# Optimization experiments

Measured on AMD Instinct MI355X. Metric: run time of the kernel, lower is better.

The kernel has to match this reference:

```python
import jax, jax.numpy as jnp
import numpy as np

N_NODES = 50000
N_EDGES = 800000
IN_DIM = 256
OUT_DIM = 64
HEADS = 4
NEG_SLOPE = 0.2  # PyG GATConv default


def setup_inputs() -> dict:
    key = jax.random.key(0)
    k1, k2, k3, k4, k5, k6 = jax.random.split(key, 6)
    x = jax.random.normal(k1, (N_NODES, IN_DIM), dtype=jnp.float32)
    edge_index = jax.random.randint(k2, (2, N_EDGES), 0, N_NODES, dtype=jnp.int64)
    scale = 1.0 / np.sqrt(IN_DIM)
    W = jax.random.normal(k3, (IN_DIM, HEADS * OUT_DIM), dtype=jnp.float32) * scale
    att_src = jax.random.normal(k4, (HEADS, OUT_DIM), dtype=jnp.float32) * scale
    att_dst = jax.random.normal(k5, (HEADS, OUT_DIM), dtype=jnp.float32) * scale
    bias = jnp.zeros((HEADS * OUT_DIM,), dtype=jnp.float32)
    return {"x": x, "edge_index": edge_index, "W": W,
            "att_src": att_src, "att_dst": att_dst, "bias": bias}


def reference(x, edge_index, W, att_src, att_dst, bias):
    N = x.shape[0]
    H, C = att_src.shape
    # add self loops (PyG GATConv default add_self_loops=True)
    loop = jnp.arange(N, dtype=edge_index.dtype)
    src = jnp.concatenate([edge_index[0], loop])  # [E+N] source j
    dst = jnp.concatenate([edge_index[1], loop])  # [E+N] target i
    # linear projection, per-head features  [N, H, C]
    h = (x @ W).reshape(N, H, C)
    # attention logits: a_src . h_j + a_dst . h_i  -> [E, H]
    a_src = jnp.einsum('nhc,hc->nh', h, att_src)
    a_dst = jnp.einsum('nhc,hc->nh', h, att_dst)
    e = jax.nn.leaky_relu(a_src[src] + a_dst[dst], negative_slope=NEG_SLOPE)
    # edge softmax over incoming edges of each destination node
    m = jax.ops.segment_max(e, dst, num_segments=N)          # [N, H]
    p = jnp.exp(e - m[dst])                                  # [E, H]
    denom = jax.ops.segment_sum(p, dst, num_segments=N)      # [N, H]
    alpha = p / (denom[dst] + 1e-16)                         # [E, H]
    # weighted scatter-aggregate of gathered source features
    out = jax.ops.segment_sum(alpha[:, :, None] * h[src], dst, num_segments=N)
    out = out.reshape(N, H * C) + bias
    return jax.nn.relu(out)  # GATLayer active_func
```

## Files before the change

kernel.cpp:

```cpp
#include <hip/hip_runtime.h>

constexpr int N  = 50000;
constexpr int E  = 800000;
constexpr int K  = 256;
constexpr int F  = 256;
constexpr int H  = 4;
constexpr float SLOPE = 0.2f;

constexpr int WT_ROWS = 272;

constexpr size_t OFF_HB   = 0;
constexpr size_t OFF_WT   = OFF_HB   + (size_t)N * F * 2;
constexpr size_t OFF_ASRC = OFF_WT   + (size_t)WT_ROWS * K * 2;
constexpr size_t OFF_ADST = OFF_ASRC + (size_t)N * H * 4;
constexpr size_t OFF_DEG  = OFF_ADST + (size_t)N * H * 4;
constexpr size_t OFF_OFFS = OFF_DEG  + (size_t)N * 4;
constexpr size_t OFF_FLAG = OFF_OFFS + (size_t)(N + 16) * 4;
constexpr size_t OFF_RANK = OFF_FLAG + 64;
constexpr size_t OFF_CSR  = OFF_RANK + (size_t)E * 4;

constexpr int HIST_BLOCKS = 128;
constexpr int GEMM_BLOCKS = (N + 127) / 128;

typedef short short8 __attribute__((ext_vector_type(8)));
typedef float floatx4 __attribute__((ext_vector_type(4)));

__device__ __forceinline__ float leaky(float x) {
    return x > 0.f ? x : SLOPE * x;
}
__device__ __forceinline__ float blo(unsigned u) { return __uint_as_float(u << 16); }
__device__ __forceinline__ float bhi(unsigned u) { return __uint_as_float(u & 0xffff0000u); }
__device__ __forceinline__ unsigned short f2b(float f) {
    unsigned u = __float_as_uint(f);
    return (unsigned short)((u + 0x7fffu + ((u >> 16) & 1u)) >> 16);
}
__device__ __forceinline__ unsigned pk2(float a, float b) {
    return (unsigned)f2b(a) | ((unsigned)f2b(b) << 16);
}

__device__ __forceinline__ int edge_at(const void* ei, int is64, size_t i) {
    if (is64) return (int)((const long long*)ei)[i];
    return ((const int*)ei)[i];
}

__global__ __launch_bounds__(256)
void prep(const float* __restrict__ Wm, const float* __restrict__ att_src,
          const float* __restrict__ att_dst, const unsigned* __restrict__ ei_words,
          unsigned short* __restrict__ Wt, int* __restrict__ flag,
          int4* __restrict__ zero_region) {
    __shared__ float tile[64][65];
    const int bid = blockIdx.x;
    const int t = threadIdx.x;
    if (bid < 16) {
        const int k0 = (bid & 3) * 64;
        const int n0 = (bid >> 2) * 64;
        const int r = t >> 2;
        const int c4 = (t & 3) * 16;
        #pragma unroll
        for (int i = 0; i < 16; i += 4) {
            float4 v = *reinterpret_cast<const float4*>(
                Wm + (size_t)(k0 + r) * F + n0 + c4 + i);
            tile[r][c4 + i + 0] = v.x;
            tile[r][c4 + i + 1] = v.y;
            tile[r][c4 + i + 2] = v.z;
            tile[r][c4 + i + 3] = v.w;
        }
        __syncthreads();
        unsigned pk[8];
        #pragma unroll
        for (int j = 0; j < 8; ++j)
            pk[j] = pk2(tile[c4 + 2 * j + 0][r], tile[c4 + 2 * j + 1][r]);
        unsigned short* dst = Wt + (size_t)(n0 + r) * K + k0 + c4;
        *reinterpret_cast<uint4*>(dst)     = make_uint4(pk[0], pk[1], pk[2], pk[3]);
        *reinterpret_cast<uint4*>(dst + 8) = make_uint4(pk[4], pk[5], pk[6], pk[7]);
    } else if (bid == 16) {
        const int k = t;
        #pragma unroll
        for (int h = 0; h < H; ++h) {
            const float* wr = Wm + (size_t)k * F + h * 64;
            float s = 0.f, d = 0.f;
            #pragma unroll 8
            for (int c = 0; c < 64; ++c) {
                float w = wr[c];
                s += w * att_src[h * 64 + c];
                d += w * att_dst[h * 64 + c];
            }
            Wt[(size_t)(256 + h) * K + k] = f2b(s);
            Wt[(size_t)(260 + h) * K + k] = f2b(d);
        }
        #pragma unroll
        for (int r = 0; r < 8; ++r) Wt[(size_t)(264 + r) * K + k] = 0;
    } else if (bid == 17) {
        if (t < 64) {
            unsigned v = ei_words[2 * t + 1];
            unsigned long long b = __ballot(v != 0u);
            if (t == 0) *flag = (b == 0ull) ? 1 : 0;
        }
    } else {
        int idx = (bid - 18) * 256 + t;
        if (idx < 12500) zero_region[idx] = make_int4(0, 0, 0, 0);
    }
}

constexpr int LDA = 72;
constexpr int LDW = 72;

__global__ __launch_bounds__(512, 4)
void gemm_hist(const float* __restrict__ X, const unsigned short* __restrict__ Wt,
               unsigned short* __restrict__ Hb, float* __restrict__ asrc,
               float* __restrict__ adst, const void* __restrict__ ei,
               const int* __restrict__ flag, int* __restrict__ deg,
               unsigned* __restrict__ rankpack) {
    __shared__ unsigned short Al[128 * LDA];
    __shared__ unsigned short Wl[WT_ROWS * LDW];
    const int tid = threadIdx.x;

    if (blockIdx.x < HIST_BLOCKS) {
        const int is64 = *flag;
        for (int i = blockIdx.x * 512 + tid; i < E; i += HIST_BLOCKS * 512) {
            int d = edge_at(ei, is64, (size_t)E + i);
            int r = atomicAdd(&deg[d], 1);
            rankpack[i] = ((unsigned)r << 17) | (unsigned)d;
        }
        return;
    }

    const int wv = tid >> 6, lane = tid & 63;
    const int quad = lane >> 4, l15 = lane & 15;
    const int rH = wv >> 2;
    const int cQ = wv & 3;
    const int m0 = (blockIdx.x - HIST_BLOCKS) * 128;

    floatx4 acc[4][4];
    #pragma unroll
    for (int i = 0; i < 4; ++i)
        #pragma unroll
        for (int j = 0; j < 4; ++j) acc[i][j] = (floatx4)0.f;
    floatx4 accf[4];
    #pragma unroll
    for (int i = 0; i < 4; ++i) accf[i] = (floatx4)0.f;

    const int ar = tid >> 2;
    const int akc = (tid & 3) * 16;
    const bool arow_ok = (m0 + ar) < N;
    const int wr = tid >> 1;
    const int wkc = (tid & 1) * 32;

    for (int k0 = 0; k0 < K; k0 += 64) {
        {
            const float* src = X + (size_t)(m0 + ar) * K + k0 + akc;
            unsigned short* dst = &Al[ar * LDA + akc];
            #pragma unroll
            for (int i = 0; i < 16; i += 4) {
                float4 v = arow_ok ? *reinterpret_cast<const float4*>(src + i)
                                   : make_float4(0.f, 0.f, 0.f, 0.f);
                *reinterpret_cast<uint2*>(dst + i) =
                    make_uint2(pk2(v.x, v.y), pk2(v.z, v.w));
            }
        }
        {
            const unsigned short* src = Wt + (size_t)wr * K + k0 + wkc;
            unsigned short* dst = &Wl[wr * LDW + wkc];
            #pragma unroll
            for (int i = 0; i < 32; i += 8)
                *reinterpret_cast<int4*>(dst + i) =
                    *reinterpret_cast<const int4*>(src + i);
        }
        if (tid < 32) {
            const int fr = 256 + (tid >> 1);
            const int fk = (tid & 1) * 32;
            const unsigned short* src = Wt + (size_t)fr * K + k0 + fk;
            unsigned short* dst = &Wl[fr * LDW + fk];
            #pragma unroll
            for (int i = 0; i < 32; i += 8)
                *reinterpret_cast<int4*>(dst + i) =
                    *reinterpret_cast<const int4*>(src + i);
        }
        __syncthreads();
        #pragma unroll
        for (int kk = 0; kk < 64; kk += 32) {
            short8 a[4];
            #pragma unroll
            for (int i = 0; i < 4; ++i)
                a[i] = *reinterpret_cast<const short8*>(
                    &Al[(rH * 64 + i * 16 + l15) * LDA + kk + quad * 8]);
            #pragma unroll
            for (int j = 0; j < 4; ++j) {
                short8 b = *reinterpret_cast<const short8*>(
                    &Wl[(cQ * 64 + j * 16 + l15) * LDW + kk + quad * 8]);
                #pragma unroll
                for (int i = 0; i < 4; ++i)
                    acc[i][j] = __builtin_amdgcn_mfma_f32_16x16x32_bf16(
                        a[i], b, acc[i][j], 0, 0, 0);
            }
            if (cQ == 3) {
                short8 bf = *reinterpret_cast<const short8*>(
                    &Wl[(256 + l15) * LDW + kk + quad * 8]);
                #pragma unroll
                for (int i = 0; i < 4; ++i)
                    accf[i] = __builtin_amdgcn_mfma_f32_16x16x32_bf16(
                        a[i], bf, accf[i], 0, 0, 0);
            }
        }
        __syncthreads();
    }
    #pragma unroll
    for (int i = 0; i < 4; ++i) {
        const int rbase = m0 + rH * 64 + i * 16 + quad * 4;
        #pragma unroll
        for (int j = 0; j < 4; ++j) {
            const int col = cQ * 64 + j * 16 + l15;
            #pragma unroll
            for (int r = 0; r < 4; ++r) {
                int row = rbase + r;
                if (row < N) Hb[(size_t)row * F + col] = f2b(acc[i][j][r]);
            }
        }
    }
    if (cQ == 3) {
        #pragma unroll
        for (int i = 0; i < 4; ++i) {
            const int rbase = m0 + rH * 64 + i * 16 + quad * 4;
            #pragma unroll
            for (int r = 0; r < 4; ++r) {
                int row = rbase + r;
                if (row < N) {
                    if (l15 < 4)      asrc[row * H + l15] = accf[i][r];
                    else if (l15 < 8) adst[row * H + (l15 - 4)] = accf[i][r];
                }
            }
        }
    }
}

__global__ __launch_bounds__(1024)
void scan_deg(const int* __restrict__ deg, int* __restrict__ offs) {
    __shared__ int sums[1024];
    const int t = threadIdx.x;
    const int lo = t * 52;
    const int hi = min(lo + 52, N);
    int s = 0;
    if (lo < N) {
        const int4* p = reinterpret_cast<const int4*>(deg + lo);
        const int n4 = (hi - lo) >> 2;
        for (int i = 0; i < n4; ++i) {
            int4 v = p[i];
            s += v.x + v.y + v.z + v.w;
        }
    }
    sums[t] = s;
    __syncthreads();
    for (int off = 1; off < 1024; off <<= 1) {
        int v = (t >= off) ? sums[t - off] : 0;
        __syncthreads();
        sums[t] += v;
        __syncthreads();
    }
    int base = sums[t] - s;
    if (lo < N) {
        const int4* p = reinterpret_cast<const int4*>(deg + lo);
        int4* q = reinterpret_cast<int4*>(offs + lo);
        const int n4 = (hi - lo) >> 2;
        for (int i = 0; i < n4; ++i) {
            int4 v = p[i];
            int4 o;
            o.x = base;
            o.y = o.x + v.x;
            o.z = o.y + v.y;
            o.w = o.z + v.z;
            base = o.w + v.w;
            q[i] = o;
        }
    }
    if (t == 0) offs[N] = sums[1023];
}

__global__ void scatter_edges(const void* __restrict__ ei,
                              const int* __restrict__ flag,
                              const int* __restrict__ offs,
                              const unsigned* __restrict__ rankpack,
                              int* __restrict__ csr) {
    const int is64 = *flag;
    for (int i = blockIdx.x * blockDim.x + threadIdx.x; i < E;
         i += gridDim.x * blockDim.x) {
        unsigned pk = rankpack[i];
        int d = (int)(pk & 0x1ffffu);
        int r = (int)(pk >> 17);
        int s = edge_at(ei, is64, i);
        csr[offs[d] + r] = s;
    }
}

__global__ __launch_bounds__(256)
void aggregate(const unsigned short* __restrict__ Hb, const float* __restrict__ asrc,
               const float* __restrict__ adst, const int* __restrict__ offs,
               const int* __restrict__ csr, const float* __restrict__ bias,
               float* __restrict__ out) {
    __shared__ float part[2][64][5];
    const int wave = threadIdx.x >> 6;
    const int lane = threadIdx.x & 63;
    const int slot = wave >> 1;
    const int role = wave & 1;
    const int node = blockIdx.x * 2 + slot;
    const int hd = lane >> 4;

    const char* hbase = (const char*)Hb;
    const char* abase = (const char*)asrc;
    const unsigned lsh = (unsigned)lane << 3;
    const unsigned hsh = (unsigned)hd << 2;

    const float adsti = adst[node * H + hd];
    const int start = offs[node];
    const int end = offs[node + 1];
    const int half = (end - start) >> 1;
    const int eb = role == 0 ? start : start + half;
    const int ee = role == 0 ? start + half : end;

    float denom = 0.f;
    float ax = 0.f, ay = 0.f, az = 0.f, aw = 0.f;
    int e = eb;
    for (; e + 8 <= ee; e += 8) {
        unsigned s[8]; float l[8]; uint2 u[8]; float p[8];
        #pragma unroll
        for (int j = 0; j < 8; ++j) s[j] = (unsigned)csr[e + j];
        #pragma unroll
        for (int j = 0; j < 8; ++j)
            l[j] = *(const float*)(abase + ((s[j] << 4) + hsh));
        #pragma unroll
        for (int j = 0; j < 8; ++j)
            u[j] = *(const uint2*)(hbase + ((s[j] << 9) + lsh));
        #pragma unroll
        for (int j = 0; j < 8; ++j) {
            p[j] = __expf(leaky(l[j] + adsti));
            denom += p[j];
            ax += p[j] * blo(u[j].x);
            ay += p[j] * bhi(u[j].x);
            az += p[j] * blo(u[j].y);
            aw += p[j] * bhi(u[j].y);
        }
    }
    for (; e + 2 <= ee; e += 2) {
        unsigned s0 = (unsigned)csr[e], s1 = (unsigned)csr[e + 1];
        float l0 = *(const float*)(abase + ((s0 << 4) + hsh));
        float l1 = *(const float*)(abase + ((s1 << 4) + hsh));
        uint2 u0 = *(const uint2*)(hbase + ((s0 << 9) + lsh));
        uint2 u1 = *(const uint2*)(hbase + ((s1 << 9) + lsh));
        float p0 = __expf(leaky(l0 + adsti));
        float p1 = __expf(leaky(l1 + adsti));
        denom += p0 + p1;
        ax += p0 * blo(u0.x) + p1 * blo(u1.x);
        ay += p0 * bhi(u0.x) + p1 * bhi(u1.x);
        az += p0 * blo(u0.y) + p1 * blo(u1.y);
        aw += p0 * bhi(u0.y) + p1 * bhi(u1.y);
    }
    if (e < ee) {
        unsigned s0 = (unsigned)csr[e];
        float l0 = *(const float*)(abase + ((s0 << 4) + hsh));
        uint2 u0 = *(const uint2*)(hbase + ((s0 << 9) + lsh));
        float p0 = __expf(leaky(l0 + adsti));
        denom += p0;
        ax += p0 * blo(u0.x);
        ay += p0 * bhi(u0.x);
        az += p0 * blo(u0.y);
        aw += p0 * bhi(u0.y);
    }
    if (role == 0) {
        float asrci = *(const float*)(abase + (((unsigned)node << 4) + hsh));
        float p = __expf(leaky(asrci + adsti));
        uint2 u = *(const uint2*)(hbase + (((unsigned)node << 9) + lsh));
        denom += p;
        ax += p * blo(u.x);
        ay += p * bhi(u.x);
        az += p * blo(u.y);
        aw += p * bhi(u.y);
    } else {
        part[slot][lane][0] = ax;
        part[slot][lane][1] = ay;
        part[slot][lane][2] = az;
        part[slot][lane][3] = aw;
        part[slot][lane][4] = denom;
    }
    __syncthreads();
    if (role == 0) {
        ax += part[slot][lane][0];
        ay += part[slot][lane][1];
        az += part[slot][lane][2];
        aw += part[slot][lane][3];
        denom += part[slot][lane][4];
        const float inv = 1.f / (denom + 1e-16f);
        float4 bv = *reinterpret_cast<const float4*>(bias + lane * 4);
        float4 o;
        o.x = fmaxf(ax * inv + bv.x, 0.f);
        o.y = fmaxf(ay * inv + bv.y, 0.f);
        o.z = fmaxf(az * inv + bv.z, 0.f);
        o.w = fmaxf(aw * inv + bv.w, 0.f);
        *reinterpret_cast<float4*>(out + (size_t)node * F + lane * 4) = o;
    }
}

extern "C" void kernel_launch(void* const* d_in, const int* in_sizes, int n_in,
                              void* d_out, int out_size, void* d_ws, size_t ws_size,
                              hipStream_t stream) {
    const float* x       = (const float*)d_in[0];
    const void*  ei      = d_in[1];
    const float* Wm      = (const float*)d_in[2];
    const float* att_src = (const float*)d_in[3];
    const float* att_dst = (const float*)d_in[4];
    const float* bias    = (const float*)d_in[5];
    float* out = (float*)d_out;

    char* ws = (char*)d_ws;
    unsigned short* hb = (unsigned short*)(ws + OFF_HB);
    unsigned short* wt = (unsigned short*)(ws + OFF_WT);
    float* asrc = (float*)(ws + OFF_ASRC);
    float* adst = (float*)(ws + OFF_ADST);
    int* deg  = (int*)(ws + OFF_DEG);
    int* offs = (int*)(ws + OFF_OFFS);
    int* flag = (int*)(ws + OFF_FLAG);
    unsigned* rankpack = (unsigned*)(ws + OFF_RANK);
    int* csr  = (int*)(ws + OFF_CSR);

    prep<<<67, 256, 0, stream>>>(Wm, att_src, att_dst, (const unsigned*)ei,
                                 wt, flag, (int4*)(ws + OFF_DEG));
    gemm_hist<<<HIST_BLOCKS + GEMM_BLOCKS, 512, 0, stream>>>(
        x, wt, hb, asrc, adst, ei, flag, deg, rankpack);
    scan_deg<<<1, 1024, 0, stream>>>(deg, offs);
    scatter_edges<<<1024, 256, 0, stream>>>(ei, flag, offs, rankpack, csr);
    aggregate<<<N / 2, 256, 0, stream>>>(hb, asrc, adst, offs, csr, bias, out);
}
```

Measured before the change: 263.9 us.

## Aggregate one node per wave with half-wave edge split and shuffle reduction

The aggregation kernel now gives each wave one destination node. The two 32-lane halves process alternating edges, and each lane loads 16 bytes (8 bf16 features) per gathered row. Partial sums are combined with a cross-half shuffle instead of shared memory and __syncthreads, and the self-loop term is handled by the upper half. This removes the LDS reduction and block barrier and widens the memory accesses. In exchange each thread holds more accumulator registers, and a launch-bounds occupancy hint is added.

After: 258.9 us. About the same (-1.9%).

```diff
diff --git a/kernel.cpp b/kernel.cpp
--- a/kernel.cpp
+++ b/kernel.cpp
@@ -291,110 +291,100 @@
     }
 }
 
-__global__ __launch_bounds__(256)
+__global__ __launch_bounds__(256, 8)
 void aggregate(const unsigned short* __restrict__ Hb, const float* __restrict__ asrc,
                const float* __restrict__ adst, const int* __restrict__ offs,
                const int* __restrict__ csr, const float* __restrict__ bias,
                float* __restrict__ out) {
-    __shared__ float part[2][64][5];
-    const int wave = threadIdx.x >> 6;
+    const int wv = threadIdx.x >> 6;
     const int lane = threadIdx.x & 63;
-    const int slot = wave >> 1;
-    const int role = wave & 1;
-    const int node = blockIdx.x * 2 + slot;
-    const int hd = lane >> 4;
+    const int half = lane >> 5;
+    const int l32 = lane & 31;
+    const int hd = l32 >> 3;
+    const int node = blockIdx.x * 4 + wv;
 
     const char* hbase = (const char*)Hb;
     const char* abase = (const char*)asrc;
-    const unsigned lsh = (unsigned)lane << 3;
+    const unsigned lsh = (unsigned)l32 << 4;
     const unsigned hsh = (unsigned)hd << 2;
 
     const float adsti = adst[node * H + hd];
     const int start = offs[node];
     const int end = offs[node + 1];
-    const int half = (end - start) >> 1;
-    const int eb = role == 0 ? start : start + half;
-    const int ee = role == 0 ? start + half : end;
 
     float denom = 0.f;
-    float ax = 0.f, ay = 0.f, az = 0.f, aw = 0.f;
-    int e = eb;
-    for (; e + 8 <= ee; e += 8) {
-        unsigned s[8]; float l[8]; uint2 u[8]; float p[8];
-        #pragma unroll
-        for (int j = 0; j < 8; ++j) s[j] = (unsigned)csr[e + j];
-        #pragma unroll
-        for (int j = 0; j < 8; ++j)
+    float a0 = 0.f, a1 = 0.f, a2 = 0.f, a3 = 0.f;
+    float a4 = 0.f, a5 = 0.f, a6 = 0.f, a7 = 0.f;
+    int e = start;
+    for (; e + 8 <= end; e += 8) {
+        unsigned s[4]; float l[4]; uint4 u[4];
+        #pragma unroll
+        for (int j = 0; j < 4; ++j) s[j] = (unsigned)csr[e + 2 * j + half];
+        #pragma unroll
+        for (int j = 0; j < 4; ++j)
             l[j] = *(const float*)(abase + ((s[j] << 4) + hsh));
         #pragma unroll
-        for (int j = 0; j < 8; ++j)
-            u[j] = *(const uint2*)(hbase + ((s[j] << 9) + lsh));
-        #pragma unroll
-        for (int j = 0; j < 8; ++j) {
-            p[j] = __expf(leaky(l[j] + adsti));
-            denom += p[j];
-            ax += p[j] * blo(u[j].x);
-            ay += p[j] * bhi(u[j].x);
-            az += p[j] * blo(u[j].y);
-            aw += p[j] * bhi(u[j].y);
-        }
-    }
-    for (; e + 2 <= ee; e += 2) {
-        unsigned s0 = (unsigned)csr[e], s1 = (unsigned)csr[e + 1];
+        for (int j = 0; j < 4; ++j)
+            u[j] = *(const uint4*)(hbase + ((s[j] << 9) + lsh));
+        #pragma unroll
+        for (int j = 0; j < 4; ++j) {
+            float p = __expf(leaky(l[j] + adsti));
+            denom += p;
+            a0 += p * blo(u[j].x); a1 += p * bhi(u[j].x);
+            a2 += p * blo(u[j].y); a3 += p * bhi(u[j].y);
+            a4 += p * blo(u[j].z); a5 += p * bhi(u[j].z);
+            a6 += p * blo(u[j].w); a7 += p * bhi(u[j].w);
+        }
+    }
+    for (; e + 2 <= end; e += 2) {
+        unsigned s0 = (unsigned)csr[e + half];
         float l0 = *(const float*)(abase + ((s0 << 4) + hsh));
-        float l1 = *(const float*)(abase + ((s1 << 4) + hsh));
-        uint2 u0 = *(const uint2*)(hbase + ((s0 << 9) + lsh));
-        uint2 u1 = *(const uint2*)(hbase + ((s1 << 9) + lsh));
-        float p0 = __expf(leaky(l0 + adsti));
-        float p1 = __expf(leaky(l1 + adsti));
-        denom += p0 + p1;
-        ax += p0 * blo(u0.x) + p1 * blo(u1.x);
-        ay += p0 * bhi(u0.x) + p1 * bhi(u1.x);
-        az += p0 * blo(u0.y) + p1 * blo(u1.y);
-        aw += p0 * bhi(u0.y) + p1 * bhi(u1.y);
-    }
-    if (e < ee) {
-        unsigned s0 = (unsigned)csr[e];
-        float l0 = *(const float*)(abase + ((s0 << 4) + hsh));
-        uint2 u0 = *(const uint2*)(hbase + ((s0 << 9) + lsh));
-        float p0 = __expf(leaky(l0 + adsti));
-        denom += p0;
-        ax += p0 * blo(u0.x);
-        ay += p0 * bhi(u0.x);
-        az += p0 * blo(u0.y);
-        aw += p0 * bhi(u0.y);
-    }
-    if (role == 0) {
-        float asrci = *(const float*)(abase + (((unsigned)node << 4) + hsh));
-        float p = __expf(leaky(asrci + adsti));
-        uint2 u = *(const uint2*)(hbase + (((unsigned)node << 9) + lsh));
+        uint4 u0 = *(const uint4*)(hbase + ((s0 << 9) + lsh));
+        float p = __expf(leaky(l0 + adsti));
         denom += p;
-        ax += p * blo(u.x);
-        ay += p * bhi(u.x);
-        az += p * blo(u.y);
-        aw += p * bhi(u.y);
-    } else {
-        part[slot][lane][0] = ax;
-        part[slot][lane][1] = ay;
-        part[slot][lane][2] = az;
-        part[slot][lane][3] = aw;
-        part[slot][lane][4] = denom;
-    }
-    __syncthreads();
-    if (role == 0) {
-        ax += part[slot][lane][0];
-        ay += part[slot][lane][1];
-        az += part[slot][lane][2];
-        aw += part[slot][lane][3];
-        denom += part[slot][lane][4];
+        a0 += p * blo(u0.x); a1 += p * bhi(u0.x);
+        a2 += p * blo(u0.y); a3 += p * bhi(u0.y);
+        a4 += p * blo(u0.z); a5 += p * bhi(u0.z);
+        a6 += p * blo(u0.w); a7 += p * bhi(u0.w);
+    }
+    {
+        const int rem = end - e;
+        bool active;
+        unsigned sf;
+        if (half == 0) { active = (rem == 1); sf = active ? (unsigned)csr[e] : 0u; }
+        else           { active = true;       sf = (unsigned)node; }
+        if (active) {
+            float l0 = *(const float*)(abase + ((sf << 4) + hsh));
+            uint4 u0 = *(const uint4*)(hbase + ((sf << 9) + lsh));
+            float p = __expf(leaky(l0 + adsti));
+            denom += p;
+            a0 += p * blo(u0.x); a1 += p * bhi(u0.x);
+            a2 += p * blo(u0.y); a3 += p * bhi(u0.y);
+            a4 += p * blo(u0.z); a5 += p * bhi(u0.z);
+            a6 += p * blo(u0.w); a7 += p * bhi(u0.w);
+        }
+    }
+    a0 += __shfl_xor(a0, 32); a1 += __shfl_xor(a1, 32);
+    a2 += __shfl_xor(a2, 32); a3 += __shfl_xor(a3, 32);
+    a4 += __shfl_xor(a4, 32); a5 += __shfl_xor(a5, 32);
+    a6 += __shfl_xor(a6, 32); a7 += __shfl_xor(a7, 32);
+    denom += __shfl_xor(denom, 32);
+    if (half == 0) {
         const float inv = 1.f / (denom + 1e-16f);
-        float4 bv = *reinterpret_cast<const float4*>(bias + lane * 4);
-        float4 o;
-        o.x = fmaxf(ax * inv + bv.x, 0.f);
-        o.y = fmaxf(ay * inv + bv.y, 0.f);
-        o.z = fmaxf(az * inv + bv.z, 0.f);
-        o.w = fmaxf(aw * inv + bv.w, 0.f);
-        *reinterpret_cast<float4*>(out + (size_t)node * F + lane * 4) = o;
+        float4 b0 = *reinterpret_cast<const float4*>(bias + l32 * 8);
+        float4 b1 = *reinterpret_cast<const float4*>(bias + l32 * 8 + 4);
+        float4 o0, o1;
+        o0.x = fmaxf(a0 * inv + b0.x, 0.f);
+        o0.y = fmaxf(a1 * inv + b0.y, 0.f);
+        o0.z = fmaxf(a2 * inv + b0.z, 0.f);
+        o0.w = fmaxf(a3 * inv + b0.w, 0.f);
+        o1.x = fmaxf(a4 * inv + b1.x, 0.f);
+        o1.y = fmaxf(a5 * inv + b1.y, 0.f);
+        o1.z = fmaxf(a6 * inv + b1.z, 0.f);
+        o1.w = fmaxf(a7 * inv + b1.w, 0.f);
+        float* orow = out + (size_t)node * F + l32 * 8;
+        *reinterpret_cast<float4*>(orow)     = o0;
+        *reinterpret_cast<float4*>(orow + 4) = o1;
     }
 }
 
@@ -426,5 +416,5 @@
         x, wt, hb, asrc, adst, ei, flag, deg, rankpack);
     scan_deg<<<1, 1024, 0, stream>>>(deg, offs);
     scatter_edges<<<1024, 256, 0, stream>>>(ei, flag, offs, rankpack, csr);
-    aggregate<<<N / 2, 256, 0, stream>>>(hb, asrc, adst, offs, csr, bias, out);
-}
+    aggregate<<<N / 4, 256, 0, stream>>>(hb, asrc, adst, offs, csr, bias, out);
+}
```
